# Performance work log

Hardware: AMD Instinct MI355X
Metric: run time of the kernel (lower is better)

## Reference

```python
import jax, jax.numpy as jnp
import numpy as np

C = 256
DQK = 32  # in_dim // factor

def setup_inputs() -> dict:
    key = jax.random.key(0)
    ks = jax.random.split(key, 8)
    B, H, W = 4, 64, 64
    x = jax.random.normal(ks[0], (B, C, H, W), dtype=jnp.float32)
    s = 1.0 / np.sqrt(C)
    Wq = jax.random.normal(ks[1], (DQK, C), dtype=jnp.float32) * s
    bq = jnp.zeros((DQK,), dtype=jnp.float32)
    Wk = jax.random.normal(ks[2], (DQK, C), dtype=jnp.float32) * s
    bk = jnp.zeros((DQK,), dtype=jnp.float32)
    Wv = jax.random.normal(ks[3], (C, C), dtype=jnp.float32) * s
    bv = jnp.zeros((C,), dtype=jnp.float32)
    # torch inits gamma to 0 (which would zero most grads); use a nonzero scalar
    gamma = jnp.array([0.5], dtype=jnp.float32)
    return {"x": x, "Wq": Wq, "bq": bq, "Wk": Wk, "bk": bk,
            "Wv": Wv, "bv": bv, "gamma": gamma}

def reference(x, Wq, bq, Wk, bk, Wv, bv, gamma):
    B, Cc, H, W = x.shape
    N = H * W
    def conv1x1(w, b):
        return jnp.einsum('bchw,oc->bohw', x, w) + b[None, :, None, None]
    q = conv1x1(Wq, bq).reshape(B, -1, N)   # [B, dqk, N]
    k = conv1x1(Wk, bk).reshape(B, -1, N)   # [B, dqk, N]
    energy = jnp.einsum('bdn,bdm->bnm', q, k)          # [B, N, N]
    attention = jax.nn.softmax(energy, axis=-1)
    v = conv1x1(Wv, bv).reshape(B, Cc, N)   # [B, C, N]
    # out = bmm(v, attention^T): out[b,c,n] = sum_m v[b,c,m] * attn[b,n,m]
    out = jnp.einsum('bcm,bnm->bcn', v, attention).reshape(B, Cc, H, W)
    weighted_out = gamma[0] * out
    final = weighted_out + x
    return (final, weighted_out, attention)
```

## Files before the change

### kernel.cpp

```cpp
#include <hip/hip_runtime.h>
#include <stdint.h>

#define CC 256
#define NNq 4096

typedef float f32x4 __attribute__((ext_vector_type(4)));
typedef short bf16x8 __attribute__((ext_vector_type(8)));

#define MFMA16(a, b, c) __builtin_amdgcn_mfma_f32_16x16x32_bf16(a, b, c, 0, 0, 0)

static __device__ __forceinline__ short f2bf(float f) {
  unsigned u = __builtin_bit_cast(unsigned, f);
  u += 0x7fffu + ((u >> 16) & 1u);
  return (short)(u >> 16);
}
static __device__ __forceinline__ float bf2f(short s) {
  return __builtin_bit_cast(float, ((unsigned)(unsigned short)s) << 16);
}

#define SBAR() do { \
  __builtin_amdgcn_sched_barrier(0); \
  asm volatile("s_waitcnt lgkmcnt(0)" ::: "memory"); \
  __builtin_amdgcn_s_barrier(); \
  __builtin_amdgcn_sched_barrier(0); \
} while (0)

#define XSTR 66

__global__ __launch_bounds__(256) void proj_kernel(
    const float* __restrict__ x,
    const float* __restrict__ Wq, const float* __restrict__ bq,
    const float* __restrict__ Wk, const float* __restrict__ bk,
    const float* __restrict__ Wv, const float* __restrict__ bv,
    unsigned short* __restrict__ qh_, unsigned short* __restrict__ ql_,
    unsigned short* __restrict__ kh_, unsigned short* __restrict__ kl_,
    unsigned short* __restrict__ v5)
{
  __shared__ float xs[256 * XSTR];
  const int t = threadIdx.x;
  const int b = blockIdx.x >> 6;
  const int n0 = (blockIdx.x & 63) << 6;
  const float L2E = 1.4426950408889634f;

  const float* xb = x + ((size_t)b * CC) * NNq + n0;
#pragma unroll
  for (int i = 0; i < 16; ++i) {
    int fi = i * 256 + t;
    int c = fi >> 4, nv = (fi & 15) << 2;
    float4 v4 = *(const float4*)(xb + (size_t)c * NNq + nv);
    float* d = &xs[c * XSTR + nv];
    d[0] = v4.x; d[1] = v4.y; d[2] = v4.z; d[3] = v4.w;
  }
  __syncthreads();

  const int w = t >> 6, l = t & 63;
  const int l15 = l & 15, l4 = l >> 4;

  f32x4 acc[5][4];
#pragma unroll
  for (int r5 = 0; r5 < 5; ++r5) {
    int rt = w * 5 + r5;
    const float* bias; float bscale;
    if (rt < 16)      { bias = bv + rt * 16;        bscale = 1.f; }
    else if (rt < 18) { bias = bq + (rt - 16) * 16; bscale = L2E; }
    else              { bias = bk + (rt - 18) * 16; bscale = 1.f; }
#pragma unroll
    for (int j = 0; j < 4; ++j) {
      float bval = bias[l4 * 4 + j] * bscale;
#pragma unroll
      for (int nt = 0; nt < 4; ++nt) acc[r5][nt][j] = bval;
    }
  }

#pragma unroll 1
  for (int ks = 0; ks < 8; ++ks) {
    bf16x8 ah[5], al[5];
#pragma unroll
    for (int r5 = 0; r5 < 5; ++r5) {
      int rt = w * 5 + r5;
      const float* wrow; float wscale;
      if (rt < 16)      { wrow = Wv + (size_t)(rt * 16 + l15) * 256;        wscale = 1.f; }
      else if (rt < 18) { wrow = Wq + (size_t)((rt - 16) * 16 + l15) * 256; wscale = L2E; }
      else              { wrow = Wk + (size_t)((rt - 18) * 16 + l15) * 256; wscale = 1.f; }
      const float* src = wrow + ks * 32 + l4 * 8;
#pragma unroll
      for (int i = 0; i < 8; ++i) {
        float v = src[i] * wscale;
        short hh = f2bf(v);
        ah[r5][i] = hh;
        al[r5][i] = f2bf(v - bf2f(hh));
      }
    }
#pragma unroll
    for (int nt = 0; nt < 4; ++nt) {
      bf16x8 bh, bl;
#pragma unroll
      for (int i = 0; i < 8; ++i) {
        float v = xs[(ks * 32 + l4 * 8 + i) * XSTR + nt * 16 + l15];
        short hh = f2bf(v);
        bh[i] = hh;
        bl[i] = f2bf(v - bf2f(hh));
      }
#pragma unroll
      for (int r5 = 0; r5 < 5; ++r5) {
        acc[r5][nt] = MFMA16(ah[r5], bl, acc[r5][nt]);
        acc[r5][nt] = MFMA16(al[r5], bh, acc[r5][nt]);
        acc[r5][nt] = MFMA16(ah[r5], bh, acc[r5][nt]);
      }
    }
  }

#pragma unroll
  for (int r5 = 0; r5 < 5; ++r5) {
    int rt = w * 5 + r5;
#pragma unroll
    for (int nt = 0; nt < 4; ++nt) {
      int n = n0 + nt * 16 + l15;
#pragma unroll
      for (int j = 0; j < 4; ++j) {
        float v = acc[r5][nt][j];
        int sub = l4 * 4 + j;
        if (rt < 16) {
          int c = rt * 16 + sub;
          size_t o = (((size_t)b * 128 + (n >> 5)) * 256 + c) * 32 + (n & 31);
          v5[o] = (unsigned short)f2bf(v);
        } else {
          short hh = f2bf(v);
          short lo = f2bf(v - bf2f(hh));
          unsigned short* dh = (rt < 18) ? qh_ : kh_;
          unsigned short* dl = (rt < 18) ? ql_ : kl_;
          int d = ((rt < 18) ? (rt - 16) : (rt - 18)) * 16 + sub;
          size_t o = ((size_t)b * NNq + n) * 32 + d;
          dh[o] = (unsigned short)hh;
          dl[o] = (unsigned short)lo;
        }
      }
    }
  }
}

__global__ __launch_bounds__(512, 4) void attn_pv_kernel(
    const unsigned short* __restrict__ qh_, const unsigned short* __restrict__ ql_,
    const unsigned short* __restrict__ kh_, const unsigned short* __restrict__ kl_,
    const unsigned short* __restrict__ v5, const float* __restrict__ x,
    const float* __restrict__ gamma, float* __restrict__ out)
{
  __shared__ __align__(16) unsigned short p_lds[2][4096];
  __shared__ float sums_lds[8][32];

  const int t = threadIdx.x, w = t >> 6, l = t & 63;
  const int l15 = l & 15, l4 = l >> 4;
  const int sb = ((blockIdx.x & 7) << 6) | (blockIdx.x >> 3);
  const int b = sb >> 7;
  const int n0 = (sb & 127) << 5;

  const unsigned short* khb = kh_ + (size_t)b * NNq * 32;
  const unsigned short* klb = kl_ + (size_t)b * NNq * 32;
  const unsigned short* vbb = v5 + (size_t)b * 1048576;
  float* attn = out + 8388608 + (size_t)b * NNq * NNq + (size_t)n0 * NNq;

  bf16x8 q2h[2], q2l[2];
#pragma unroll
  for (int rg = 0; rg < 2; ++rg) {
    size_t qo = ((size_t)b * NNq + n0 + rg * 16 + l15) * 32 + l4 * 8;
    q2h[rg] = *(const bf16x8*)(qh_ + qo);
    q2l[rg] = *(const bf16x8*)(ql_ + qo);
  }

  float sx[2][4] = {{0.f,0.f,0.f,0.f},{0.f,0.f,0.f,0.f}};
  {
    const int mq = w * 512;
    bf16x8 kch[2], kcl[2];
#pragma unroll
    for (int mt = 0; mt < 2; ++mt) {
      size_t ko = (size_t)(mq + mt * 16 + l15) * 32 + l4 * 8;
      kch[mt] = *(const bf16x8*)(khb + ko);
      kcl[mt] = *(const bf16x8*)(klb + ko);
    }
#pragma unroll 1
    for (int it = 0; it < 16; ++it) {
      const int nx = mq + ((it + 1) & 15) * 32;
      bf16x8 knh[2], knl[2];
#pragma unroll
      for (int mt = 0; mt < 2; ++mt) {
        size_t ko = (size_t)(nx + mt * 16 + l15) * 32 + l4 * 8;
        knh[mt] = *(const bf16x8*)(khb + ko);
        knl[mt] = *(const bf16x8*)(klb + ko);
      }
#pragma unroll
      for (int mt = 0; mt < 2; ++mt) {
#pragma unroll
        for (int rg = 0; rg < 2; ++rg) {
          f32x4 e = {0.f, 0.f, 0.f, 0.f};
          e = MFMA16(q2h[rg], kcl[mt], e);
          e = MFMA16(q2l[rg], kch[mt], e);
          e = MFMA16(q2h[rg], kch[mt], e);
#pragma unroll
          for (int j = 0; j < 4; ++j) sx[rg][j] += exp2f(e[j] - 64.0f);
        }
      }
      kch[0] = knh[0]; kch[1] = knh[1];
      kcl[0] = knl[0]; kcl[1] = knl[1];
    }
  }
#pragma unroll
  for (int mask = 1; mask < 16; mask <<= 1)
#pragma unroll
    for (int rg = 0; rg < 2; ++rg)
#pragma unroll
      for (int j = 0; j < 4; ++j) sx[rg][j] += __shfl_xor(sx[rg][j], mask);
  if (l15 == 0) {
#pragma unroll
    for (int rg = 0; rg < 2; ++rg)
#pragma unroll
      for (int j = 0; j < 4; ++j)
        sums_lds[w][rg * 16 + l4 * 4 + j] = sx[rg][j];
  }
  __syncthreads();

  if (w < 4) {
    const int g = w >> 1, h = w & 1;
    const bf16x8 qh = q2h[g], qlo = q2l[g];
    f32x4 crow;
#pragma unroll
    for (int j = 0; j < 4; ++j) {
      int r = g * 16 + l4 * 4 + j;
      float S = 0.f;
#pragma unroll
      for (int ww = 0; ww < 8; ++ww) S += sums_lds[ww][r];
      crow[j] = 64.0f + log2f(S);
    }

    bf16x8 kAh[4], kAl[4];
    bf16x8 pwv[2];

    auto loadK = [&](int chunk, bf16x8 (&KH)[4], bf16x8 (&KL)[4]) {
#pragma unroll
      for (int sub = 0; sub < 4; ++sub) {
        size_t ko = (size_t)(chunk * 128 + h * 64 + sub * 16 + l15) * 32 + l4 * 8;
        KH[sub] = *(const bf16x8*)(khb + ko);
        KL[sub] = *(const bf16x8*)(klb + ko);
      }
    };
    auto estep = [&](int ec, const bf16x8 (&KH)[4], const bf16x8 (&KL)[4]) {
#pragma unroll
      for (int sub = 0; sub < 4; ++sub) {
        f32x4 e = {0.f, 0.f, 0.f, 0.f};
        e = MFMA16(qh, KL[sub], e);
        e = MFMA16(qlo, KH[sub], e);
        e = MFMA16(qh, KH[sub], e);
#pragma unroll
        for (int j = 0; j < 4; ++j) {
          float p = exp2f(e[j] - crow[j]);
          int nl = g * 16 + l4 * 4 + j;
          int ml = h * 64 + sub * 16 + l15;
          __builtin_nontemporal_store(p, attn + (size_t)nl * NNq + ec * 128 + ml);
          pwv[sub >> 1][(sub & 1) * 4 + j] = f2bf(p);
        }
      }
    };
    auto pwrite = [&](int par) {
      char* pld = (char*)p_lds[par];
#pragma unroll
      for (int sub = 0; sub < 4; ++sub)
#pragma unroll
        for (int j = 0; j < 4; ++j) {
          int nl = g * 16 + l4 * 4 + j;
          int ml = h * 64 + sub * 16 + l15;
          int byteo = nl * 256 + ((ml * 2) ^ ((nl & 7) << 4));
          *(unsigned short*)(pld + byteo) =
              (unsigned short)pwv[sub >> 1][(sub & 1) * 4 + j];
        }
    };

    loadK(0, kAh, kAl);
    estep(0, kAh, kAl);
    pwrite(0);
    loadK(1, kAh, kAl);

#pragma unroll 1
    for (int it = 0; it < 32; ++it) {
      bf16x8 kBh[4], kBl[4];
      loadK((it + 2) & 31, kBh, kBl);
      if (it < 31) estep(it + 1, kAh, kAl);
      SBAR();
      if (it < 31) pwrite((it + 1) & 1);
#pragma unroll
      for (int sub = 0; sub < 4; ++sub) { kAh[sub] = kBh[sub]; kAl[sub] = kBl[sub]; }
    }
  } else {
    const int cw = w - 4;
    f32x4 acc[4][2];
#pragma unroll
    for (int ct = 0; ct < 4; ++ct)
#pragma unroll
      for (int nt = 0; nt < 2; ++nt) acc[ct][nt] = f32x4{0.f, 0.f, 0.f, 0.f};

    bf16x8 vf[4][4];
    auto vload = [&](int chunk) {
#pragma unroll
      for (int ct = 0; ct < 4; ++ct)
#pragma unroll
        for (int ms = 0; ms < 4; ++ms) {
          size_t vo = (size_t)(chunk * 4 + ms) * 8192 +
                      (size_t)(cw * 64 + ct * 16 + l15) * 32 + l4 * 8;
          vf[ct][ms] = *(const bf16x8*)(vbb + vo);
        }
    };
    vload(0);

#pragma unroll 1
    for (int it = 0; it < 32; ++it) {
      SBAR();
      char* pl = (char*)p_lds[it & 1];
      __builtin_amdgcn_s_setprio(1);
#pragma unroll
      for (int ms = 0; ms < 4; ++ms) {
        int mbyte = ms * 64 + l4 * 16;
        int o0 = l15 * 256 + (mbyte ^ ((l15 & 7) << 4));
        int o1 = (16 + l15) * 256 + (mbyte ^ (((16 + l15) & 7) << 4));
        bf16x8 pf0 = *(const bf16x8*)(pl + o0);
        bf16x8 pf1 = *(const bf16x8*)(pl + o1);
#pragma unroll
        for (int ct = 0; ct < 4; ++ct) {
          acc[ct][0] = MFMA16(vf[ct][ms], pf0, acc[ct][0]);
          acc[ct][1] = MFMA16(vf[ct][ms], pf1, acc[ct][1]);
        }
      }
      __builtin_amdgcn_s_setprio(0);
      if (it < 31) vload(it + 1);
    }

    const float gm = gamma[0];
#pragma unroll
    for (int ct = 0; ct < 4; ++ct) {
#pragma unroll
      for (int nt = 0; nt < 2; ++nt) {
#pragma unroll
        for (int j = 0; j < 4; ++j) {
          int c = cw * 64 + ct * 16 + l4 * 4 + j;
          int n = n0 + nt * 16 + l15;
          size_t go = ((size_t)b * CC + c) * NNq + n;
          float o = acc[ct][nt][j] * gm;
          out[4194304 + go] = o;
          out[go] = o + x[go];
        }
      }
    }
  }
}

extern "C" void kernel_launch(void* const* d_in, const int* in_sizes, int n_in,
                              void* d_out, int out_size, void* d_ws, size_t ws_size,
                              hipStream_t stream) {
  const float* x     = (const float*)d_in[0];
  const float* Wq    = (const float*)d_in[1];
  const float* bq    = (const float*)d_in[2];
  const float* Wk    = (const float*)d_in[3];
  const float* bk    = (const float*)d_in[4];
  const float* Wv    = (const float*)d_in[5];
  const float* bv    = (const float*)d_in[6];
  const float* gamma = (const float*)d_in[7];
  float* out = (float*)d_out;

  char* ws = (char*)d_ws;
  unsigned short* qh   = (unsigned short*)(ws);
  unsigned short* ql   = (unsigned short*)(ws + (1u << 20));
  unsigned short* kh   = (unsigned short*)(ws + (2u << 20));
  unsigned short* kl   = (unsigned short*)(ws + (3u << 20));
  unsigned short* v5   = (unsigned short*)(ws + (4u << 20));

  proj_kernel<<<256, 256, 0, stream>>>(x, Wq, bq, Wk, bk, Wv, bv, qh, ql, kh, kl, v5);
  attn_pv_kernel<<<512, 512, 0, stream>>>(qh, ql, kh, kl, v5, x, gamma, out);
}
```

Baseline: 151.9 us.

## Double attention query tile to 64 rows with 1024-thread blocks

Each block of the fused attention/PV kernel now handles 64 query rows instead of 32, with 16 waves: 8 produce softmax probabilities and 8 run the PV accumulation. Each PV wave now covers 32 channels across 64 query columns. Grid size is halved, so each streamed K and V tile is reused by twice as many rows and global K/V traffic is cut. In exchange, per-block LDS and register pressure rise, and with 256 blocks there is only one block per CU, so there is less latency hiding across blocks.

```diff
diff --git a/kernel.cpp b/kernel.cpp
--- a/kernel.cpp
+++ b/kernel.cpp
@@ -139,37 +139,41 @@
   }
 }
 
-__global__ __launch_bounds__(512, 4) void attn_pv_kernel(
+__global__ __launch_bounds__(1024, 4) void attn_pv_kernel(
     const unsigned short* __restrict__ qh_, const unsigned short* __restrict__ ql_,
     const unsigned short* __restrict__ kh_, const unsigned short* __restrict__ kl_,
     const unsigned short* __restrict__ v5, const float* __restrict__ x,
     const float* __restrict__ gamma, float* __restrict__ out)
 {
-  __shared__ __align__(16) unsigned short p_lds[2][4096];
-  __shared__ float sums_lds[8][32];
+  __shared__ __align__(16) unsigned short p_lds[2][8192];
+  __shared__ float sums_lds[16][64];
 
   const int t = threadIdx.x, w = t >> 6, l = t & 63;
   const int l15 = l & 15, l4 = l >> 4;
-  const int sb = ((blockIdx.x & 7) << 6) | (blockIdx.x >> 3);
-  const int b = sb >> 7;
-  const int n0 = (sb & 127) << 5;
+  const int sb = ((blockIdx.x & 7) << 5) | (blockIdx.x >> 3);
+  const int b = sb >> 6;
+  const int n0 = (sb & 63) << 6;
 
   const unsigned short* khb = kh_ + (size_t)b * NNq * 32;
   const unsigned short* klb = kl_ + (size_t)b * NNq * 32;
   const unsigned short* vbb = v5 + (size_t)b * 1048576;
   float* attn = out + 8388608 + (size_t)b * NNq * NNq + (size_t)n0 * NNq;
 
-  bf16x8 q2h[2], q2l[2];
-#pragma unroll
-  for (int rg = 0; rg < 2; ++rg) {
+  bf16x8 q4h[4], q4l[4];
+#pragma unroll
+  for (int rg = 0; rg < 4; ++rg) {
     size_t qo = ((size_t)b * NNq + n0 + rg * 16 + l15) * 32 + l4 * 8;
-    q2h[rg] = *(const bf16x8*)(qh_ + qo);
-    q2l[rg] = *(const bf16x8*)(ql_ + qo);
-  }
-
-  float sx[2][4] = {{0.f,0.f,0.f,0.f},{0.f,0.f,0.f,0.f}};
+    q4h[rg] = *(const bf16x8*)(qh_ + qo);
+    q4l[rg] = *(const bf16x8*)(ql_ + qo);
+  }
+
+  float sx[4][4];
+#pragma unroll
+  for (int rg = 0; rg < 4; ++rg)
+#pragma unroll
+    for (int j = 0; j < 4; ++j) sx[rg][j] = 0.f;
   {
-    const int mq = w * 512;
+    const int mq = w * 256;
     bf16x8 kch[2], kcl[2];
 #pragma unroll
     for (int mt = 0; mt < 2; ++mt) {
@@ -178,8 +182,8 @@
       kcl[mt] = *(const bf16x8*)(klb + ko);
     }
 #pragma unroll 1
-    for (int it = 0; it < 16; ++it) {
-      const int nx = mq + ((it + 1) & 15) * 32;
+    for (int it = 0; it < 8; ++it) {
+      const int nx = mq + ((it + 1) & 7) * 32;
       bf16x8 knh[2], knl[2];
 #pragma unroll
       for (int mt = 0; mt < 2; ++mt) {
@@ -190,11 +194,11 @@
 #pragma unroll
       for (int mt = 0; mt < 2; ++mt) {
 #pragma unroll
-        for (int rg = 0; rg < 2; ++rg) {
+        for (int rg = 0; rg < 4; ++rg) {
           f32x4 e = {0.f, 0.f, 0.f, 0.f};
-          e = MFMA16(q2h[rg], kcl[mt], e);
-          e = MFMA16(q2l[rg], kch[mt], e);
-          e = MFMA16(q2h[rg], kch[mt], e);
+          e = MFMA16(q4h[rg], kcl[mt], e);
+          e = MFMA16(q4l[rg], kch[mt], e);
+          e = MFMA16(q4h[rg], kch[mt], e);
 #pragma unroll
           for (int j = 0; j < 4; ++j) sx[rg][j] += exp2f(e[j] - 64.0f);
         }
@@ -206,28 +210,28 @@
 #pragma unroll
   for (int mask = 1; mask < 16; mask <<= 1)
 #pragma unroll
-    for (int rg = 0; rg < 2; ++rg)
+    for (int rg = 0; rg < 4; ++rg)
 #pragma unroll
       for (int j = 0; j < 4; ++j) sx[rg][j] += __shfl_xor(sx[rg][j], mask);
   if (l15 == 0) {
 #pragma unroll
-    for (int rg = 0; rg < 2; ++rg)
+    for (int rg = 0; rg < 4; ++rg)
 #pragma unroll
       for (int j = 0; j < 4; ++j)
         sums_lds[w][rg * 16 + l4 * 4 + j] = sx[rg][j];
   }
   __syncthreads();
 
-  if (w < 4) {
+  if (w < 8) {
     const int g = w >> 1, h = w & 1;
-    const bf16x8 qh = q2h[g], qlo = q2l[g];
+    const bf16x8 qh = q4h[g], qlo = q4l[g];
     f32x4 crow;
 #pragma unroll
     for (int j = 0; j < 4; ++j) {
       int r = g * 16 + l4 * 4 + j;
       float S = 0.f;
 #pragma unroll
-      for (int ww = 0; ww < 8; ++ww) S += sums_lds[ww][r];
+      for (int ww = 0; ww < 16; ++ww) S += sums_lds[ww][r];
       crow[j] = 64.0f + log2f(S);
     }
 
@@ -289,21 +293,21 @@
       for (int sub = 0; sub < 4; ++sub) { kAh[sub] = kBh[sub]; kAl[sub] = kBl[sub]; }
     }
   } else {
-    const int cw = w - 4;
-    f32x4 acc[4][2];
-#pragma unroll
-    for (int ct = 0; ct < 4; ++ct)
-#pragma unroll
-      for (int nt = 0; nt < 2; ++nt) acc[ct][nt] = f32x4{0.f, 0.f, 0.f, 0.f};
-
-    bf16x8 vf[4][4];
+    const int cw = w - 8;
+    f32x4 acc[2][4];
+#pragma unroll
+    for (int ct = 0; ct < 2; ++ct)
+#pragma unroll
+      for (int nt = 0; nt < 4; ++nt) acc[ct][nt] = f32x4{0.f, 0.f, 0.f, 0.f};
+
+    bf16x8 vf[2][4];
     auto vload = [&](int chunk) {
 #pragma unroll
-      for (int ct = 0; ct < 4; ++ct)
+      for (int ct = 0; ct < 2; ++ct)
 #pragma unroll
         for (int ms = 0; ms < 4; ++ms) {
           size_t vo = (size_t)(chunk * 4 + ms) * 8192 +
-                      (size_t)(cw * 64 + ct * 16 + l15) * 32 + l4 * 8;
+                      (size_t)(cw * 32 + ct * 16 + l15) * 32 + l4 * 8;
           vf[ct][ms] = *(const bf16x8*)(vbb + vo);
         }
     };
@@ -317,15 +321,17 @@
 #pragma unroll
       for (int ms = 0; ms < 4; ++ms) {
         int mbyte = ms * 64 + l4 * 16;
-        int o0 = l15 * 256 + (mbyte ^ ((l15 & 7) << 4));
-        int o1 = (16 + l15) * 256 + (mbyte ^ (((16 + l15) & 7) << 4));
-        bf16x8 pf0 = *(const bf16x8*)(pl + o0);
-        bf16x8 pf1 = *(const bf16x8*)(pl + o1);
-#pragma unroll
-        for (int ct = 0; ct < 4; ++ct) {
-          acc[ct][0] = MFMA16(vf[ct][ms], pf0, acc[ct][0]);
-          acc[ct][1] = MFMA16(vf[ct][ms], pf1, acc[ct][1]);
-        }
+        bf16x8 pf[4];
+#pragma unroll
+        for (int nt = 0; nt < 4; ++nt) {
+          int nl = nt * 16 + l15;
+          pf[nt] = *(const bf16x8*)(pl + nl * 256 + (mbyte ^ ((nl & 7) << 4)));
+        }
+#pragma unroll
+        for (int ct = 0; ct < 2; ++ct)
+#pragma unroll
+          for (int nt = 0; nt < 4; ++nt)
+            acc[ct][nt] = MFMA16(vf[ct][ms], pf[nt], acc[ct][nt]);
       }
       __builtin_amdgcn_s_setprio(0);
       if (it < 31) vload(it + 1);
@@ -333,12 +339,12 @@
 
     const float gm = gamma[0];
 #pragma unroll
-    for (int ct = 0; ct < 4; ++ct) {
-#pragma unroll
-      for (int nt = 0; nt < 2; ++nt) {
+    for (int ct = 0; ct < 2; ++ct) {
+#pragma unroll
+      for (int nt = 0; nt < 4; ++nt) {
 #pragma unroll
         for (int j = 0; j < 4; ++j) {
-          int c = cw * 64 + ct * 16 + l4 * 4 + j;
+          int c = cw * 32 + ct * 16 + l4 * 4 + j;
           int n = n0 + nt * 16 + l15;
           size_t go = ((size_t)b * CC + c) * NNq + n;
           float o = acc[ct][nt][j] * gm;
@@ -371,5 +377,5 @@
   unsigned short* v5   = (unsigned short*)(ws + (4u << 20));
 
   proj_kernel<<<256, 256, 0, stream>>>(x, Wq, bq, Wk, bk, Wv, bv, qh, ql, kh, kl, v5);
-  attn_pv_kernel<<<512, 512, 0, stream>>>(qh, ql, kh, kl, v5, x, gamma, out);
-}
+  attn_pv_kernel<<<256, 1024, 0, stream>>>(qh, ql, kh, kl, v5, x, gamma, out);
+}
```

Result: faster. 149.0 us, median of 2 (-2.0%).
